# Performance work log

Hardware: AMD Instinct MI355X
Metric: run time of the kernel (lower is better)

The kernel has to match this reference:

```python
import jax, jax.numpy as jnp
import numpy as np
import math

B_, L_, D_ = 1, 1024, 2048
ED, N, DCONV, DTR = 4096, 16, 4, 128


def setup_inputs() -> dict:
    key = jax.random.key(0)
    ks = jax.random.split(key, 10)
    s = lambda fan_in: 1.0 / math.sqrt(fan_in)
    x = jax.random.normal(ks[0], (B_, L_, D_), jnp.float32)
    norm_w = jnp.ones((D_,), jnp.float32)
    W_in = jax.random.uniform(ks[1], (2 * ED, D_), jnp.float32, -s(D_), s(D_))
    conv_w = jax.random.uniform(ks[2], (ED, 1, DCONV), jnp.float32, -s(DCONV), s(DCONV))
    conv_b = jax.random.uniform(ks[3], (ED,), jnp.float32, -s(DCONV), s(DCONV))
    W_x = jax.random.uniform(ks[4], (DTR + 2 * N, ED), jnp.float32, -s(ED), s(ED))
    W_dt = jax.random.uniform(ks[5], (ED, DTR), jnp.float32, -s(DTR), s(DTR))
    # dt bias init as in the module
    dt = jnp.exp(jax.random.uniform(ks[6], (ED,), jnp.float32) * (math.log(0.1) - math.log(0.001)) + math.log(0.1))
    dt = jnp.clip(dt, 1e-4, None)
    b_dt = dt + jnp.log(-jnp.expm1(-dt))
    # A = -exp(log(arange(1..N))) = -(1..N) broadcast over ED
    A = -jnp.tile(jnp.arange(1, N + 1, dtype=jnp.float32)[None, :], (ED, 1))
    D = jnp.ones((ED,), jnp.float32)
    W_out = jax.random.uniform(ks[7], (D_, ED), jnp.float32, -s(ED), s(ED))
    return {"x": x, "norm_w": norm_w, "W_in": W_in, "conv_w": conv_w, "conv_b": conv_b,
            "W_x": W_x, "W_dt": W_dt, "b_dt": b_dt, "A": A, "D": D, "W_out": W_out}


def _mamba_fwd(x, norm_w, W_in, conv_w, conv_b, W_x, W_dt, b_dt, A, D, W_out):
    # RMSNorm (module uses no eps in the sqrt)
    u = x * jax.lax.rsqrt(jnp.mean(x * x, axis=-1, keepdims=True)) * norm_w
    xz = u @ W_in.T                      # (B, L, 2*ED)
    xc, z = jnp.split(xz, 2, axis=-1)
    # causal depthwise conv1d (torch pads d_conv-1 both sides then slices [:L])
    xt = xc.transpose(0, 2, 1)           # (B, ED, L)
    conv = jax.lax.conv_general_dilated(xt, conv_w, (1,), [(DCONV - 1, 0)],
                                        feature_group_count=ED)
    conv = conv + conv_b[None, :, None]
    xs = jax.nn.silu(conv.transpose(0, 2, 1))   # (B, L, ED)
    dBC = xs @ W_x.T                     # (B, L, DTR + 2N)
    dt_lr = dBC[..., :DTR]
    Bm = dBC[..., DTR:DTR + N]           # (B, L, N)
    Cm = dBC[..., DTR + N:]              # (B, L, N)
    dt = jax.nn.softplus(dt_lr @ W_dt.T + b_dt)  # (B, L, ED)
    dA = jnp.exp(dt[..., None] * A)                       # (B, L, ED, N)
    dBx = dt[..., None] * Bm[:, :, None, :] * xs[..., None]  # (B, L, ED, N)
    h0 = jnp.zeros((x.shape[0], ED, N), x.dtype)

    def step(h, inp):
        dA_t, dBx_t, C_t = inp
        h = dA_t * h + dBx_t             # (B, ED, N)
        y_t = jnp.einsum('bdn,bn->bd', h, C_t)
        return h, y_t

    _, ys = jax.lax.scan(step, h0, (dA.transpose(1, 0, 2, 3),
                                    dBx.transpose(1, 0, 2, 3),
                                    Cm.transpose(1, 0, 2)))
    y = ys.transpose(1, 0, 2) + xs * D   # (B, L, ED)
    out = (y * jax.nn.silu(z)) @ W_out.T
    return out + x                        # residual


def reference(x, norm_w, W_in, conv_w, conv_b, W_x, W_dt, b_dt, A, D, W_out):
    return _mamba_fwd(x, norm_w, W_in, conv_w, conv_b, W_x, W_dt, b_dt, A, D, W_out)
```

## Files before the change

kernel.cpp:

```cpp
#include <hip/hip_runtime.h>
#include <cstdint>
#include <cmath>

typedef __bf16 bf16x8_t __attribute__((ext_vector_type(8)));
typedef float  f32x4_t  __attribute__((ext_vector_type(4)));

#define DEV_INLINE __device__ __forceinline__

DEV_INLINE float bf2f(unsigned short u) {
  union { uint32_t i; float f; } v; v.i = ((uint32_t)u) << 16; return v.f;
}
DEV_INLINE unsigned short f2bf(float f) {
  union { float f; uint32_t i; } v; v.f = f;
  uint32_t x = v.i;
  return (unsigned short)((x + 0x7fffu + ((x >> 16) & 1u)) >> 16);
}
DEV_INLINE float ldin(const void* p, size_t i, int fl) {
  return fl ? bf2f(((const unsigned short*)p)[i]) : ((const float*)p)[i];
}
DEV_INLINE void async_cp16(const void* g, void* l) {
  __builtin_amdgcn_global_load_lds(
      (const __attribute__((address_space(1))) uint32_t*)g,
      (__attribute__((address_space(3))) uint32_t*)l, 16, 0, 0);
}

static constexpr int L_  = 1024;
static constexpr int Dm  = 2048;
static constexpr int ED_ = 4096;
static constexpr int NST = 16;
static constexpr int NX  = 160;
static constexpr int DTRc = 128;
static constexpr int SEG = 64;
static constexpr int TSEG = L_ / SEG;
static constexpr int SKZ = 16;

__global__ __launch_bounds__(256) void detect_k(const uint32_t* __restrict__ x,
                                                int* __restrict__ flag) {
  const int tid = threadIdx.x;
  int cnt = 0;
#pragma unroll
  for (int k = 0; k < 4; ++k) {
    const uint32_t w = x[tid * 4 + k];
    const uint32_t e = (w >> 7) & 0xffu;
    cnt += (e >= 112u && e <= 143u) ? 1 : 0;
  }
#pragma unroll
  for (int o = 32; o > 0; o >>= 1) cnt += __shfl_xor(cnt, o);
  __shared__ int sc[4];
  if ((tid & 63) == 0) sc[tid >> 6] = cnt;
  __syncthreads();
  if (tid == 0) flag[0] = ((sc[0] + sc[1] + sc[2] + sc[3]) >= 600) ? 1 : 0;
}

__global__ __launch_bounds__(256) void canon4_k(
    const void* s0, const void* s1, const void* s2, const void* s3,
    unsigned short* d0, unsigned short* d1, unsigned short* d2, unsigned short* d3,
    int b1, int b2, int b3, int b4, const int* __restrict__ flag) {
  if (flag[0]) return;
  const int i = blockIdx.x * 256 + threadIdx.x;
  if (i >= b4) return;
  const float4* src; unsigned short* dst; int base;
  if (i < b1)      { src = (const float4*)s0; dst = d0; base = 0;  }
  else if (i < b2) { src = (const float4*)s1; dst = d1; base = b1; }
  else if (i < b3) { src = (const float4*)s2; dst = d2; base = b2; }
  else             { src = (const float4*)s3; dst = d3; base = b3; }
  const int j = i - base;
  const float4 a = src[2 * j], b = src[2 * j + 1];
  uint4 o;
  o.x = (uint32_t)f2bf(a.x) | ((uint32_t)f2bf(a.y) << 16);
  o.y = (uint32_t)f2bf(a.z) | ((uint32_t)f2bf(a.w) << 16);
  o.z = (uint32_t)f2bf(b.x) | ((uint32_t)f2bf(b.y) << 16);
  o.w = (uint32_t)f2bf(b.z) | ((uint32_t)f2bf(b.w) << 16);
  ((uint4*)dst)[j] = o;
}

__global__ __launch_bounds__(256) void rmsnorm_k(
    const void* __restrict__ x, const void* __restrict__ w,
    const int* __restrict__ flag, unsigned short* __restrict__ u) {
  const int row = blockIdx.x, tid = threadIdx.x;
  const int fl = flag[0];
  const size_t r0 = (size_t)row * Dm;
  float vals[8]; float ss = 0.f;
#pragma unroll
  for (int k = 0; k < 8; ++k) {
    float f = ldin(x, r0 + tid + k * 256, fl);
    vals[k] = f; ss += f * f;
  }
#pragma unroll
  for (int o = 32; o > 0; o >>= 1) ss += __shfl_xor(ss, o);
  __shared__ float sred[4];
  if ((tid & 63) == 0) sred[tid >> 6] = ss;
  __syncthreads();
  const float tot = sred[0] + sred[1] + sred[2] + sred[3];
  const float scale = rsqrtf(tot * (1.0f / Dm));
#pragma unroll
  for (int k = 0; k < 8; ++k) {
    int c = tid + k * 256;
    u[r0 + c] = f2bf(vals[k] * scale * ldin(w, c, fl));
  }
}

enum { EPI_F32 = 0, EPI_SOFTPLUS_BF16 = 1, EPI_BF16 = 2 };

template <int BM, int BN, int WTM, int WTN, int EPI>
__global__ __launch_bounds__(256) void gemm_bt(
    const unsigned short* __restrict__ A, const unsigned short* __restrict__ Bc,
    const void* __restrict__ Braw, void* __restrict__ Cv,
    const void* __restrict__ aux_raw, const int* __restrict__ flag,
    int M, int N, int K, int Kchunk) {
  constexpr int WAVES_N = BN / (16 * WTN);
  constexpr int WAVES_M = BM / (16 * WTM);
  static_assert(WAVES_M * WAVES_N == 4, "need 4 waves");
  constexpr int ATILE = BM * 32;
  constexpr int BTILE = BN * 32;
  __shared__ __align__(16) unsigned short As[ATILE];
  __shared__ __align__(16) unsigned short Bs[BTILE];

  const int fl = flag[0];
  const unsigned short* B = fl ? (const unsigned short*)Braw : Bc;

  const int tid = threadIdx.x;
  const int lane = tid & 63;
  const int w = tid >> 6;
  const int wr = (w / WAVES_N) * (WTM * 16);
  const int wc = (w % WAVES_N) * (WTN * 16);
  const int n0 = blockIdx.x * BN;
  const int m0 = blockIdx.y * BM;
  const int koff = blockIdx.z * Kchunk;
  const int lm = lane & 15;
  const int quad = lane >> 4;

  f32x4_t acc[WTM][WTN];
#pragma unroll
  for (int i = 0; i < WTM; ++i)
#pragma unroll
    for (int j = 0; j < WTN; ++j) acc[i][j] = (f32x4_t){0.f, 0.f, 0.f, 0.f};

  for (int k0 = koff; k0 < koff + Kchunk; k0 += 32) {
#pragma unroll
    for (int off = 0; off < ATILE; off += 2048) {
      const int idx = off + tid * 8;
      if (ATILE % 2048 == 0 || idx < ATILE)
        async_cp16(A + (size_t)(m0 + (idx >> 5)) * K + k0 + (idx & 31), As + idx);
    }
#pragma unroll
    for (int off = 0; off < BTILE; off += 2048) {
      const int idx = off + tid * 8;
      if (BTILE % 2048 == 0 || idx < BTILE)
        async_cp16(B + (size_t)(n0 + (idx >> 5)) * K + k0 + (idx & 31), Bs + idx);
    }
    __syncthreads();

    bf16x8_t af[WTM], bfr[WTN];
#pragma unroll
    for (int i = 0; i < WTM; ++i)
      af[i] = *(const bf16x8_t*)(As + (wr + i * 16 + lm) * 32 + quad * 8);
#pragma unroll
    for (int j = 0; j < WTN; ++j)
      bfr[j] = *(const bf16x8_t*)(Bs + (wc + j * 16 + lm) * 32 + quad * 8);
#pragma unroll
    for (int i = 0; i < WTM; ++i)
#pragma unroll
      for (int j = 0; j < WTN; ++j)
        acc[i][j] = __builtin_amdgcn_mfma_f32_16x16x32_bf16(af[i], bfr[j], acc[i][j], 0, 0, 0);
    __syncthreads();
  }

  const size_t zoff = (size_t)blockIdx.z * M * N;
#pragma unroll
  for (int i = 0; i < WTM; ++i) {
    const int row = m0 + wr + i * 16 + quad * 4;
#pragma unroll
    for (int j = 0; j < WTN; ++j) {
      const int col = n0 + wc + j * 16 + lm;
#pragma unroll
      for (int r = 0; r < 4; ++r) {
        const size_t o = zoff + (size_t)(row + r) * N + col;
        const float v = acc[i][j][r];
        if constexpr (EPI == EPI_F32) {
          ((float*)Cv)[o] = v;
        } else if constexpr (EPI == EPI_BF16) {
          ((unsigned short*)Cv)[o] = f2bf(v);
        } else {
          const float s = v + ldin(aux_raw, col, fl);
          ((unsigned short*)Cv)[o] = f2bf((s > 20.f) ? s : log1pf(__expf(s)));
        }
      }
    }
  }
}

__global__ __launch_bounds__(256) void conv_silu_k(
    const unsigned short* __restrict__ xz, const void* __restrict__ cw,
    const void* __restrict__ cb, const int* __restrict__ flag,
    unsigned short* __restrict__ xsb) {
  const int idx = blockIdx.x * 256 + threadIdx.x;
  const int d4 = idx & 1023;
  const int t = idx >> 10;
  const int d = d4 * 4;
  const int fl = flag[0];
  float a0 = ldin(cb, d + 0, fl), a1 = ldin(cb, d + 1, fl);
  float a2 = ldin(cb, d + 2, fl), a3 = ldin(cb, d + 3, fl);
#pragma unroll
  for (int j = 0; j < 4; ++j) {
    const int tt = t - 3 + j;
    if (tt >= 0) {
      const ushort4 v = *(const ushort4*)(xz + (size_t)tt * (2 * ED_) + d);
      a0 += ldin(cw, (d + 0) * 4 + j, fl) * bf2f(v.x);
      a1 += ldin(cw, (d + 1) * 4 + j, fl) * bf2f(v.y);
      a2 += ldin(cw, (d + 2) * 4 + j, fl) * bf2f(v.z);
      a3 += ldin(cw, (d + 3) * 4 + j, fl) * bf2f(v.w);
    }
  }
  const float s0 = a0 / (1.f + __expf(-a0));
  const float s1 = a1 / (1.f + __expf(-a1));
  const float s2 = a2 / (1.f + __expf(-a2));
  const float s3 = a3 / (1.f + __expf(-a3));
  ushort4 o;
  o.x = f2bf(s0); o.y = f2bf(s1); o.z = f2bf(s2); o.w = f2bf(s3);
  *(ushort4*)(xsb + (size_t)t * ED_ + d) = o;
}

__global__ __launch_bounds__(192) void dbc_fin(
    const float* __restrict__ part, unsigned short* __restrict__ dtlr,
    float* __restrict__ BC) {
  const int t = blockIdx.x, c = threadIdx.x;
  if (c >= NX) return;
  float s = 0.f;
#pragma unroll
  for (int z = 0; z < SKZ; ++z) s += part[(size_t)z * (L_ * NX) + t * NX + c];
  if (c < DTRc) dtlr[t * DTRc + c] = f2bf(s);
  else          BC[t * 32 + (c - DTRc)] = s;
}

DEV_INLINE void pow_tree(float r, float* rp) {
  rp[0] = r;
  rp[1] = rp[0] * rp[0];
  rp[2] = rp[1] * rp[0];  rp[3] = rp[1] * rp[1];
  rp[4] = rp[3] * rp[0];  rp[5] = rp[3] * rp[1];
  rp[6] = rp[3] * rp[2];  rp[7] = rp[3] * rp[3];
  rp[8]  = rp[7] * rp[0]; rp[9]  = rp[7] * rp[1];
  rp[10] = rp[7] * rp[2]; rp[11] = rp[7] * rp[3];
  rp[12] = rp[7] * rp[4]; rp[13] = rp[7] * rp[5];
  rp[14] = rp[7] * rp[6]; rp[15] = rp[7] * rp[7];
}

__global__ __launch_bounds__(256) void scan_p1(
    const unsigned short* __restrict__ dt, const unsigned short* __restrict__ xs,
    const float* __restrict__ BC, float* __restrict__ qbuf,
    float* __restrict__ dtsum) {
  const int d = blockIdx.x * 256 + threadIdx.x;
  const int s = blockIdx.y;
  const int t0 = s * TSEG;
  float h[16];
#pragma unroll
  for (int n = 0; n < 16; ++n) h[n] = 0.f;
  float dsum = 0.f;
#pragma unroll 2
  for (int tl = 0; tl < TSEG; ++tl) {
    const size_t t = t0 + tl;
    const float dtv = bf2f(dt[t * ED_ + d]);
    const float xv = bf2f(xs[t * ED_ + d]);
    const float* bc = BC + t * 32;
    float Bv[16];
    *(float4*)&Bv[0]  = *(const float4*)(bc + 0);
    *(float4*)&Bv[4]  = *(const float4*)(bc + 4);
    *(float4*)&Bv[8]  = *(const float4*)(bc + 8);
    *(float4*)&Bv[12] = *(const float4*)(bc + 12);
    dsum += dtv;
    float rp[16];
    pow_tree(__expf(-dtv), rp);
    const float dtx = dtv * xv;
#pragma unroll
    for (int n = 0; n < 16; ++n) h[n] = rp[n] * h[n] + dtx * Bv[n];
  }
  dtsum[(size_t)s * ED_ + d] = dsum;
  float* qp = qbuf + ((size_t)s * ED_ + d) * 16;
#pragma unroll
  for (int k = 0; k < 4; ++k) *(float4*)(qp + 4 * k) = *(float4*)&h[4 * k];
}

__global__ __launch_bounds__(256) void scan_p2(
    const float* __restrict__ dtsum, float* __restrict__ qbuf) {
  const int idx = blockIdx.x * 256 + threadIdx.x;
  const int d = idx >> 4, n = idx & 15;
  const float nn = -(float)(n + 1);
  float h = 0.f;
  for (int s = 0; s < SEG; ++s) {
    const size_t o = (size_t)s * (ED_ * 16) + idx;
    const float q = qbuf[o];
    const float P = __expf(nn * dtsum[(size_t)s * ED_ + d]);
    qbuf[o] = h;
    h = P * h + q;
  }
}

__global__ __launch_bounds__(256) void scan_p3(
    const unsigned short* __restrict__ dt, const unsigned short* __restrict__ xs,
    const float* __restrict__ BC, const float* __restrict__ hin,
    const void* __restrict__ Draw, const int* __restrict__ flag,
    const unsigned short* __restrict__ xz, unsigned short* __restrict__ g) {
  const int d = blockIdx.x * 256 + threadIdx.x;
  const int s = blockIdx.y;
  const int t0 = s * TSEG;
  float h[16];
  const float* hp = hin + ((size_t)s * ED_ + d) * 16;
#pragma unroll
  for (int k = 0; k < 4; ++k) *(float4*)&h[4 * k] = *(const float4*)(hp + 4 * k);
  const float Dd = ldin(Draw, d, flag[0]);
#pragma unroll 2
  for (int tl = 0; tl < TSEG; ++tl) {
    const size_t t = t0 + tl;
    const float dtv = bf2f(dt[t * ED_ + d]);
    const float xv = bf2f(xs[t * ED_ + d]);
    const float zv = bf2f(xz[t * (2 * ED_) + ED_ + d]);
    const float* bc = BC + t * 32;
    float Bv[16], Cw[16];
    *(float4*)&Bv[0]  = *(const float4*)(bc + 0);
    *(float4*)&Bv[4]  = *(const float4*)(bc + 4);
    *(float4*)&Bv[8]  = *(const float4*)(bc + 8);
    *(float4*)&Bv[12] = *(const float4*)(bc + 12);
    *(float4*)&Cw[0]  = *(const float4*)(bc + 16);
    *(float4*)&Cw[4]  = *(const float4*)(bc + 20);
    *(float4*)&Cw[8]  = *(const float4*)(bc + 24);
    *(float4*)&Cw[12] = *(const float4*)(bc + 28);
    float rp[16];
    pow_tree(__expf(-dtv), rp);
    const float dtx = dtv * xv;
    float y0 = 0.f, y1 = 0.f, y2 = 0.f, y3 = 0.f;
#pragma unroll
    for (int n = 0; n < 4; ++n) {
      h[n]    = rp[n]    * h[n]    + dtx * Bv[n];    y0 += h[n]    * Cw[n];
      h[n+4]  = rp[n+4]  * h[n+4]  + dtx * Bv[n+4];  y1 += h[n+4]  * Cw[n+4];
      h[n+8]  = rp[n+8]  * h[n+8]  + dtx * Bv[n+8];  y2 += h[n+8]  * Cw[n+8];
      h[n+12] = rp[n+12] * h[n+12] + dtx * Bv[n+12]; y3 += h[n+12] * Cw[n+12];
    }
    const float y = (y0 + y1) + (y2 + y3) + xv * Dd;
    const float sz = zv / (1.f + __expf(-zv));
    g[t * ED_ + d] = f2bf(y * sz);
  }
}

__global__ __launch_bounds__(256) void res_fin(
    const float* __restrict__ part, const void* __restrict__ xraw,
    const int* __restrict__ flag, void* __restrict__ out) {
  const int i4 = blockIdx.x * 256 + threadIdx.x;
  const float4 a = ((const float4*)part)[i4];
  const float4 b = ((const float4*)(part + (size_t)L_ * Dm))[i4];
  if (flag[0]) {
    const ushort4 xv = ((const ushort4*)xraw)[i4];
    ushort4 o;
    o.x = f2bf(a.x + b.x + bf2f(xv.x));
    o.y = f2bf(a.y + b.y + bf2f(xv.y));
    o.z = f2bf(a.z + b.z + bf2f(xv.z));
    o.w = f2bf(a.w + b.w + bf2f(xv.w));
    ((ushort4*)out)[i4] = o;
  } else {
    const float4 xv = ((const float4*)xraw)[i4];
    float4 o;
    o.x = a.x + b.x + xv.x; o.y = a.y + b.y + xv.y;
    o.z = a.z + b.z + xv.z; o.w = a.w + b.w + xv.w;
    ((float4*)out)[i4] = o;
  }
}

extern "C" void kernel_launch(void* const* d_in, const int* in_sizes, int n_in,
                              void* d_out, int out_size, void* d_ws, size_t ws_size,
                              hipStream_t stream) {
  const void* x_raw     = d_in[0];
  const void* normw_raw = d_in[1];
  const void* W_in_raw  = d_in[2];
  const void* convw_raw = d_in[3];
  const void* convb_raw = d_in[4];
  const void* W_x_raw   = d_in[5];
  const void* W_dt_raw  = d_in[6];
  const void* b_dt_raw  = d_in[7];
  const void* D_raw     = d_in[9];
  const void* W_out_raw = d_in[10];

  char* ws = (char*)d_ws;
  size_t off = 0;
  auto alloc = [&](size_t bytes) {
    void* p = ws + off; off += (bytes + 255) & ~(size_t)255; return p;
  };
  int*            flag   = (int*)alloc(256);
  unsigned short* W_in_c = (unsigned short*)alloc((size_t)in_sizes[2] * 2);
  unsigned short* W_x_c  = (unsigned short*)alloc((size_t)in_sizes[5] * 2);
  unsigned short* W_dt_c = (unsigned short*)alloc((size_t)in_sizes[6] * 2);
  unsigned short* W_out_c= (unsigned short*)alloc((size_t)in_sizes[10] * 2);
  unsigned short* u      = (unsigned short*)alloc((size_t)L_ * Dm * 2);
  unsigned short* xzb    = (unsigned short*)alloc((size_t)L_ * 2 * ED_ * 2);
  unsigned short* xsb    = (unsigned short*)alloc((size_t)L_ * ED_ * 2);
  float*          dbc_p  = (float*)alloc((size_t)SKZ * L_ * NX * 4);
  unsigned short* dtlr   = (unsigned short*)alloc((size_t)L_ * DTRc * 2);
  float*          BC     = (float*)alloc((size_t)L_ * 32 * 4);
  unsigned short* dtf    = (unsigned short*)alloc((size_t)L_ * ED_ * 2);
  float*          qbuf   = (float*)alloc((size_t)SEG * ED_ * NST * 4);
  float*          dts    = (float*)alloc((size_t)SEG * ED_ * 4);
  unsigned short* g      = (unsigned short*)alloc((size_t)L_ * ED_ * 2);
  float*          res_p  = (float*)alloc((size_t)2 * L_ * Dm * 4);

  detect_k<<<1, 256, 0, stream>>>((const uint32_t*)x_raw, flag);

  const int b1 = in_sizes[2] / 8;
  const int b2 = b1 + in_sizes[5] / 8;
  const int b3 = b2 + in_sizes[6] / 8;
  const int b4 = b3 + in_sizes[10] / 8;
  canon4_k<<<(b4 + 255) / 256, 256, 0, stream>>>(
      W_in_raw, W_x_raw, W_dt_raw, W_out_raw,
      W_in_c, W_x_c, W_dt_c, W_out_c, b1, b2, b3, b4, flag);

  rmsnorm_k<<<L_, 256, 0, stream>>>(x_raw, normw_raw, flag, u);

  gemm_bt<64, 128, 4, 2, EPI_BF16><<<dim3(64, 16, 1), 256, 0, stream>>>(
      u, W_in_c, W_in_raw, xzb, nullptr, flag, L_, 2 * ED_, Dm, Dm);

  conv_silu_k<<<(L_ * ED_ / 4) / 256, 256, 0, stream>>>(
      xzb, convw_raw, convb_raw, flag, xsb);

  gemm_bt<64, 32, 1, 2, EPI_F32><<<dim3(NX / 32, L_ / 64, SKZ), 256, 0, stream>>>(
      xsb, W_x_c, W_x_raw, dbc_p, nullptr, flag, L_, NX, ED_, ED_ / SKZ);
  dbc_fin<<<L_, 192, 0, stream>>>(dbc_p, dtlr, BC);

  gemm_bt<64, 64, 2, 2, EPI_SOFTPLUS_BF16><<<dim3(ED_ / 64, L_ / 64, 1), 256, 0, stream>>>(
      dtlr, W_dt_c, W_dt_raw, dtf, b_dt_raw, flag, L_, ED_, DTRc, DTRc);

  scan_p1<<<dim3(ED_ / 256, SEG), 256, 0, stream>>>(dtf, xsb, BC, qbuf, dts);
  scan_p2<<<(ED_ * NST) / 256, 256, 0, stream>>>(dts, qbuf);
  scan_p3<<<dim3(ED_ / 256, SEG), 256, 0, stream>>>(dtf, xsb, BC, qbuf, D_raw, flag, xzb, g);

  gemm_bt<64, 64, 2, 2, EPI_F32><<<dim3(Dm / 64, L_ / 64, 2), 256, 0, stream>>>(
      g, W_out_c, W_out_raw, res_p, nullptr, flag, L_, Dm, ED_, 2048);
  res_fin<<<(L_ * Dm / 4) / 256, 256, 0, stream>>>(res_p, x_raw, flag, d_out);
}
```

Before: 364.4 us.

## Fuse fp32-to-bf16 weight conversion into GEMM B-tile loads and retile split-K GEMMs

Removes the separate weight canonicalisation kernel and instead converts fp32 weights to bf16 on the fly while loading B tiles into LDS inside each GEMM, using synchronous float4 loads in place of async LDS copies. It also retiles the W_x GEMM to a single 160-wide N tile with split-K doubled to 32, and the W_out GEMM to 128-wide tiles with split-K 4, with res_fin summing four partials. This avoids one pass over roughly 100MB of fp32 weights and the matching bf16 write, at the cost of repeated per-tile conversion, non-async B loads and larger partial-sum buffers.

```diff
diff --git a/kernel.cpp b/kernel.cpp
--- a/kernel.cpp
+++ b/kernel.cpp
@@ -32,7 +32,7 @@
 static constexpr int DTRc = 128;
 static constexpr int SEG = 64;
 static constexpr int TSEG = L_ / SEG;
-static constexpr int SKZ = 16;
+static constexpr int SKZ = 32;
 
 __global__ __launch_bounds__(256) void detect_k(const uint32_t* __restrict__ x,
                                                 int* __restrict__ flag) {
@@ -50,28 +50,6 @@
   if ((tid & 63) == 0) sc[tid >> 6] = cnt;
   __syncthreads();
   if (tid == 0) flag[0] = ((sc[0] + sc[1] + sc[2] + sc[3]) >= 600) ? 1 : 0;
-}
-
-__global__ __launch_bounds__(256) void canon4_k(
-    const void* s0, const void* s1, const void* s2, const void* s3,
-    unsigned short* d0, unsigned short* d1, unsigned short* d2, unsigned short* d3,
-    int b1, int b2, int b3, int b4, const int* __restrict__ flag) {
-  if (flag[0]) return;
-  const int i = blockIdx.x * 256 + threadIdx.x;
-  if (i >= b4) return;
-  const float4* src; unsigned short* dst; int base;
-  if (i < b1)      { src = (const float4*)s0; dst = d0; base = 0;  }
-  else if (i < b2) { src = (const float4*)s1; dst = d1; base = b1; }
-  else if (i < b3) { src = (const float4*)s2; dst = d2; base = b2; }
-  else             { src = (const float4*)s3; dst = d3; base = b3; }
-  const int j = i - base;
-  const float4 a = src[2 * j], b = src[2 * j + 1];
-  uint4 o;
-  o.x = (uint32_t)f2bf(a.x) | ((uint32_t)f2bf(a.y) << 16);
-  o.y = (uint32_t)f2bf(a.z) | ((uint32_t)f2bf(a.w) << 16);
-  o.z = (uint32_t)f2bf(b.x) | ((uint32_t)f2bf(b.y) << 16);
-  o.w = (uint32_t)f2bf(b.z) | ((uint32_t)f2bf(b.w) << 16);
-  ((uint4*)dst)[j] = o;
 }
 
 __global__ __launch_bounds__(256) void rmsnorm_k(
@@ -104,10 +82,9 @@
 
 template <int BM, int BN, int WTM, int WTN, int EPI>
 __global__ __launch_bounds__(256) void gemm_bt(
-    const unsigned short* __restrict__ A, const unsigned short* __restrict__ Bc,
-    const void* __restrict__ Braw, void* __restrict__ Cv,
-    const void* __restrict__ aux_raw, const int* __restrict__ flag,
-    int M, int N, int K, int Kchunk) {
+    const unsigned short* __restrict__ A, const void* __restrict__ Braw,
+    void* __restrict__ Cv, const void* __restrict__ aux_raw,
+    const int* __restrict__ flag, int M, int N, int K, int Kchunk) {
   constexpr int WAVES_N = BN / (16 * WTN);
   constexpr int WAVES_M = BM / (16 * WTM);
   static_assert(WAVES_M * WAVES_N == 4, "need 4 waves");
@@ -117,7 +94,8 @@
   __shared__ __align__(16) unsigned short Bs[BTILE];
 
   const int fl = flag[0];
-  const unsigned short* B = fl ? (const unsigned short*)Braw : Bc;
+  const unsigned short* Bb = (const unsigned short*)Braw;
+  const float*          Bf = (const float*)Braw;
 
   const int tid = threadIdx.x;
   const int lane = tid & 63;
@@ -143,11 +121,29 @@
       if (ATILE % 2048 == 0 || idx < ATILE)
         async_cp16(A + (size_t)(m0 + (idx >> 5)) * K + k0 + (idx & 31), As + idx);
     }
-#pragma unroll
-    for (int off = 0; off < BTILE; off += 2048) {
-      const int idx = off + tid * 8;
-      if (BTILE % 2048 == 0 || idx < BTILE)
-        async_cp16(B + (size_t)(n0 + (idx >> 5)) * K + k0 + (idx & 31), Bs + idx);
+    if (fl) {
+#pragma unroll
+      for (int off = 0; off < BTILE; off += 2048) {
+        const int idx = off + tid * 8;
+        if (BTILE % 2048 == 0 || idx < BTILE)
+          async_cp16(Bb + (size_t)(n0 + (idx >> 5)) * K + k0 + (idx & 31), Bs + idx);
+      }
+    } else {
+#pragma unroll
+      for (int off = 0; off < BTILE; off += 2048) {
+        const int idx = off + tid * 8;
+        if (BTILE % 2048 == 0 || idx < BTILE) {
+          const float* gp = Bf + (size_t)(n0 + (idx >> 5)) * K + k0 + (idx & 31);
+          const float4 f0 = *(const float4*)(gp);
+          const float4 f1 = *(const float4*)(gp + 4);
+          uint4 o;
+          o.x = (uint32_t)f2bf(f0.x) | ((uint32_t)f2bf(f0.y) << 16);
+          o.y = (uint32_t)f2bf(f0.z) | ((uint32_t)f2bf(f0.w) << 16);
+          o.z = (uint32_t)f2bf(f1.x) | ((uint32_t)f2bf(f1.y) << 16);
+          o.w = (uint32_t)f2bf(f1.z) | ((uint32_t)f2bf(f1.w) << 16);
+          *(uint4*)(Bs + idx) = o;
+        }
+      }
     }
     __syncthreads();
 
@@ -345,21 +341,25 @@
     const float* __restrict__ part, const void* __restrict__ xraw,
     const int* __restrict__ flag, void* __restrict__ out) {
   const int i4 = blockIdx.x * 256 + threadIdx.x;
-  const float4 a = ((const float4*)part)[i4];
-  const float4 b = ((const float4*)(part + (size_t)L_ * Dm))[i4];
+  float4 a = ((const float4*)part)[i4];
+#pragma unroll
+  for (int z = 1; z < 4; ++z) {
+    const float4 b = ((const float4*)(part + (size_t)z * L_ * Dm))[i4];
+    a.x += b.x; a.y += b.y; a.z += b.z; a.w += b.w;
+  }
   if (flag[0]) {
     const ushort4 xv = ((const ushort4*)xraw)[i4];
     ushort4 o;
-    o.x = f2bf(a.x + b.x + bf2f(xv.x));
-    o.y = f2bf(a.y + b.y + bf2f(xv.y));
-    o.z = f2bf(a.z + b.z + bf2f(xv.z));
-    o.w = f2bf(a.w + b.w + bf2f(xv.w));
+    o.x = f2bf(a.x + bf2f(xv.x));
+    o.y = f2bf(a.y + bf2f(xv.y));
+    o.z = f2bf(a.z + bf2f(xv.z));
+    o.w = f2bf(a.w + bf2f(xv.w));
     ((ushort4*)out)[i4] = o;
   } else {
     const float4 xv = ((const float4*)xraw)[i4];
     float4 o;
-    o.x = a.x + b.x + xv.x; o.y = a.y + b.y + xv.y;
-    o.z = a.z + b.z + xv.z; o.w = a.w + b.w + xv.w;
+    o.x = a.x + xv.x; o.y = a.y + xv.y;
+    o.z = a.z + xv.z; o.w = a.w + xv.w;
     ((float4*)out)[i4] = o;
   }
 }
@@ -384,10 +384,6 @@
     void* p = ws + off; off += (bytes + 255) & ~(size_t)255; return p;
   };
   int*            flag   = (int*)alloc(256);
-  unsigned short* W_in_c = (unsigned short*)alloc((size_t)in_sizes[2] * 2);
-  unsigned short* W_x_c  = (unsigned short*)alloc((size_t)in_sizes[5] * 2);
-  unsigned short* W_dt_c = (unsigned short*)alloc((size_t)in_sizes[6] * 2);
-  unsigned short* W_out_c= (unsigned short*)alloc((size_t)in_sizes[10] * 2);
   unsigned short* u      = (unsigned short*)alloc((size_t)L_ * Dm * 2);
   unsigned short* xzb    = (unsigned short*)alloc((size_t)L_ * 2 * ED_ * 2);
   unsigned short* xsb    = (unsigned short*)alloc((size_t)L_ * ED_ * 2);
@@ -398,38 +394,30 @@
   float*          qbuf   = (float*)alloc((size_t)SEG * ED_ * NST * 4);
   float*          dts    = (float*)alloc((size_t)SEG * ED_ * 4);
   unsigned short* g      = (unsigned short*)alloc((size_t)L_ * ED_ * 2);
-  float*          res_p  = (float*)alloc((size_t)2 * L_ * Dm * 4);
+  float*          res_p  = (float*)alloc((size_t)4 * L_ * Dm * 4);
 
   detect_k<<<1, 256, 0, stream>>>((const uint32_t*)x_raw, flag);
 
-  const int b1 = in_sizes[2] / 8;
-  const int b2 = b1 + in_sizes[5] / 8;
-  const int b3 = b2 + in_sizes[6] / 8;
-  const int b4 = b3 + in_sizes[10] / 8;
-  canon4_k<<<(b4 + 255) / 256, 256, 0, stream>>>(
-      W_in_raw, W_x_raw, W_dt_raw, W_out_raw,
-      W_in_c, W_x_c, W_dt_c, W_out_c, b1, b2, b3, b4, flag);
-
   rmsnorm_k<<<L_, 256, 0, stream>>>(x_raw, normw_raw, flag, u);
 
   gemm_bt<64, 128, 4, 2, EPI_BF16><<<dim3(64, 16, 1), 256, 0, stream>>>(
-      u, W_in_c, W_in_raw, xzb, nullptr, flag, L_, 2 * ED_, Dm, Dm);
+      u, W_in_raw, xzb, nullptr, flag, L_, 2 * ED_, Dm, Dm);
 
   conv_silu_k<<<(L_ * ED_ / 4) / 256, 256, 0, stream>>>(
       xzb, convw_raw, convb_raw, flag, xsb);
 
-  gemm_bt<64, 32, 1, 2, EPI_F32><<<dim3(NX / 32, L_ / 64, SKZ), 256, 0, stream>>>(
-      xsb, W_x_c, W_x_raw, dbc_p, nullptr, flag, L_, NX, ED_, ED_ / SKZ);
+  gemm_bt<64, 160, 2, 5, EPI_F32><<<dim3(1, L_ / 64, SKZ), 256, 0, stream>>>(
+      xsb, W_x_raw, dbc_p, nullptr, flag, L_, NX, ED_, ED_ / SKZ);
   dbc_fin<<<L_, 192, 0, stream>>>(dbc_p, dtlr, BC);
 
   gemm_bt<64, 64, 2, 2, EPI_SOFTPLUS_BF16><<<dim3(ED_ / 64, L_ / 64, 1), 256, 0, stream>>>(
-      dtlr, W_dt_c, W_dt_raw, dtf, b_dt_raw, flag, L_, ED_, DTRc, DTRc);
+      dtlr, W_dt_raw, dtf, b_dt_raw, flag, L_, ED_, DTRc, DTRc);
 
   scan_p1<<<dim3(ED_ / 256, SEG), 256, 0, stream>>>(dtf, xsb, BC, qbuf, dts);
   scan_p2<<<(ED_ * NST) / 256, 256, 0, stream>>>(dts, qbuf);
   scan_p3<<<dim3(ED_ / 256, SEG), 256, 0, stream>>>(dtf, xsb, BC, qbuf, D_raw, flag, xzb, g);
 
-  gemm_bt<64, 64, 2, 2, EPI_F32><<<dim3(Dm / 64, L_ / 64, 2), 256, 0, stream>>>(
-      g, W_out_c, W_out_raw, res_p, nullptr, flag, L_, Dm, ED_, 2048);
+  gemm_bt<64, 128, 4, 2, EPI_F32><<<dim3(Dm / 128, L_ / 64, 4), 256, 0, stream>>>(
+      g, W_out_raw, res_p, nullptr, flag, L_, Dm, ED_, ED_ / 4);
   res_fin<<<(L_ * Dm / 4) / 256, 256, 0, stream>>>(res_p, x_raw, flag, d_out);
 }
```

New measurement: 386.2 us. 1.06x slower.
